# Optimization experiments

Hardware: AMD Instinct MI355X
Metric: run time of the kernel (lower is better)

Reference implementation:

```python
import jax, jax.numpy as jnp
import numpy as np

NEG_INF = -1e9
ROUTING_ITERS = 3


def squash(z):
    # z: [B, K, D]
    norm_sq = jnp.sum(z * z, axis=-1, keepdims=True)
    norm = jnp.sqrt(norm_sq + 1e-8)
    return norm_sq / (1.0 + norm_sq) * (z / norm)


def setup_inputs() -> dict:
    key = jax.random.key(0)
    k1, k2, k3, k4 = jax.random.split(key, 4)
    B, L, D, K = 2048, 200, 256, 8
    behavior_embeds = jax.random.normal(k1, (B, L, D), dtype=jnp.float32)
    W = jax.random.normal(k2, (D, D), dtype=jnp.float32) * (1.0 / np.sqrt(D))
    b_init = jax.random.normal(k3, (B, K, L), dtype=jnp.float32)
    mask = jax.random.randint(k4, (B, L), 0, 2, dtype=jnp.int32)
    return {"behavior_embeds": behavior_embeds, "W": W, "b_init": b_init, "mask": mask}


def reference(behavior_embeds, W, b_init, mask):
    # behavior_embeds: [B, L, D]; W: [D, D] (nn.Linear weight, y = x @ W.T)
    u_hat = jnp.einsum('bld,ed->ble', behavior_embeds, W)  # [B, L, D]
    # mask padding positions in routing logits
    b = jnp.where(mask[:, None, :] == 0, NEG_INF, b_init)  # [B, K, L]
    c = None
    for i in range(ROUTING_ITERS):
        w = jax.nn.softmax(b, axis=2)                      # [B, K, L]
        z = jnp.einsum('bkl,bld->bkd', w, u_hat)           # [B, K, D]
        c = squash(z)
        if i < ROUTING_ITERS - 1:
            b = b + jnp.einsum('bkd,bld->bkl', c, u_hat)
    return c
```

## Files before the change

### kernel.cpp

```cpp
#include <hip/hip_runtime.h>
#include <hip/hip_bf16.h>

#define B_ 2048
#define L_ 200
#define D_ 256
#define K_ 8

typedef __attribute__((ext_vector_type(8))) _Float16 half8;
typedef __attribute__((ext_vector_type(4))) _Float16 half4v;
typedef __attribute__((ext_vector_type(4))) float f32x4;

#define LTP 232
#define WP  232
#define CP  264

#define OFF_UTT  0
#define OFF_WH   118784
#define OFF_WL   126208
#define OFF_CH   133632
#define OFF_CL   142080
#define OFF_LB   150528
#define OFF_RED  156928
#define OFF_SC   157440
#define LDS_TOTAL 157472

__global__ __launch_bounds__(256) void w_to_f16(const float* __restrict__ W,
                                                _Float16* __restrict__ Wh) {
    const int idx = (blockIdx.x * 256 + threadIdx.x) * 4;
    const float4 v = *(const float4*)(W + idx);
    half4v h = { (_Float16)v.x, (_Float16)v.y, (_Float16)v.z, (_Float16)v.w };
    *(half4v*)(Wh + idx) = h;
}

__global__ __launch_bounds__(1024) void fused_mie(
        const float* __restrict__ X, const float* __restrict__ b_init,
        const int* __restrict__ mask, const _Float16* __restrict__ Wh,
        float* __restrict__ out) {
    extern __shared__ char dyn[];
    _Float16* utT = (_Float16*)(dyn + OFF_UTT);
    _Float16* wHs = (_Float16*)(dyn + OFF_WH);
    _Float16* wLs = (_Float16*)(dyn + OFF_WL);
    _Float16* cHs = (_Float16*)(dyn + OFF_CH);
    _Float16* cLs = (_Float16*)(dyn + OFF_CL);
    _Float16* Us  = (_Float16*)(dyn + OFF_CH);
    _Float16* Xs  = (_Float16*)(dyn + OFF_CL);
    float* lb   = (float*)(dyn + OFF_LB);
    float* red2 = (float*)(dyn + OFF_RED);
    float* scS  = (float*)(dyn + OFF_SC);

    const int b = blockIdx.x;
    const int t = threadIdx.x;
    const int w = t >> 6, lane = t & 63;
    const int fr = lane & 15, hi = lane >> 4;

    {
        const int row = t >> 2, part = t & 3;
        *(int4*)&utT[row * LTP + 200 + 8 * part] = make_int4(0, 0, 0, 0);
    }
    if (t < 928) *(int4*)(dyn + OFF_WH + 16 * t) = make_int4(0, 0, 0, 0);
    for (int idx = t; idx < K_ * L_; idx += 1024) {
        const int k = idx / L_, l = idx - k * L_;
        lb[idx] = (mask[b * L_ + l] == 0) ? -1e9f
                                          : b_init[(size_t)b * (K_ * L_) + idx];
    }

    half8 bw[8];
    {
        const _Float16* wr = Wh + (size_t)(16 * w + fr) * 256;
#pragma unroll
        for (int d0 = 0; d0 < 8; ++d0)
            bw[d0] = *(const half8*)(wr + 32 * d0 + 8 * hi);
    }

    const float* Xb = X + (size_t)b * L_ * D_;
    const int sc4 = lane * 4;
    {
        const float4 v = *(const float4*)(Xb + w * 256 + sc4);
        half4v h = { (_Float16)v.x, (_Float16)v.y, (_Float16)v.z, (_Float16)v.w };
        *(half4v*)&Xs[w * CP + sc4] = h;
    }
    __syncthreads();

    half8 au[8];
    for (int lt = 0; lt < 13; ++lt) {
        f32x4 acc = {};
#pragma unroll
        for (int d0 = 0; d0 < 8; ++d0) {
            const half8 a8 = *(const half8*)&Xs[fr * CP + 32 * d0 + 8 * hi];
            acc = __builtin_amdgcn_mfma_f32_16x16x32_f16(a8, bw[d0], acc, 0, 0, 0);
        }
        float4 xv = make_float4(0.f, 0.f, 0.f, 0.f);
        if (lt < 12) {
            const int l = 16 * (lt + 1) + w;
            if (l < L_) xv = *(const float4*)(Xb + l * 256 + sc4);
        }
#pragma unroll
        for (int j = 0; j < 4; ++j)
            Us[(4 * hi + j) * CP + 16 * w + fr] = (_Float16)acc[j];
        __syncthreads();
        if (w == lt) {
#pragma unroll
            for (int d0 = 0; d0 < 8; ++d0)
                au[d0] = *(const half8*)&Us[fr * CP + 32 * d0 + 8 * hi];
        }
        {
            const int c = t & 255, r0 = (t >> 8) * 4;
            half4v p = { Us[(r0 + 0) * CP + c], Us[(r0 + 1) * CP + c],
                         Us[(r0 + 2) * CP + c], Us[(r0 + 3) * CP + c] };
            *(half4v*)&utT[c * LTP + 16 * lt + r0] = p;
        }
        if (lt < 12) {
            half4v h = { (_Float16)xv.x, (_Float16)xv.y, (_Float16)xv.z, (_Float16)xv.w };
            *(half4v*)&Xs[w * CP + sc4] = h;
        }
        __syncthreads();
    }

    for (int iter = 0; iter < 3; ++iter) {
        if (t < 512) {
            const int k = t >> 6, ln = t & 63;
            float v[4];
            float m = -1e30f;
#pragma unroll
            for (int i = 0; i < 4; ++i) {
                const int l = ln + 64 * i;
                v[i] = (l < L_) ? lb[k * L_ + l] : -1e30f;
                m = fmaxf(m, v[i]);
            }
#pragma unroll
            for (int off = 32; off >= 1; off >>= 1)
                m = fmaxf(m, __shfl_xor(m, off));
            float e[4], s = 0.f;
#pragma unroll
            for (int i = 0; i < 4; ++i) {
                const int l = ln + 64 * i;
                e[i] = (l < L_) ? __expf(v[i] - m) : 0.f;
                s += e[i];
            }
#pragma unroll
            for (int off = 32; off >= 1; off >>= 1)
                s += __shfl_xor(s, off);
            const float rinv = 1.0f / s;
#pragma unroll
            for (int i = 0; i < 4; ++i) {
                const int l = ln + 64 * i;
                if (l < L_) {
                    const float wv = e[i] * rinv;
                    const _Float16 h = (_Float16)wv;
                    wHs[k * WP + l] = h;
                    wLs[k * WP + l] = (_Float16)(wv - (float)h);
                }
            }
        }
        __syncthreads();

        f32x4 zac = {};
#pragma unroll
        for (int ks = 0; ks < 7; ++ks) {
            const half8 bz = *(const half8*)&utT[(16 * w + fr) * LTP + 32 * ks + 8 * hi];
            const half8 ah = *(const half8*)&wHs[fr * WP + 32 * ks + 8 * hi];
            const half8 al = *(const half8*)&wLs[fr * WP + 32 * ks + 8 * hi];
            zac = __builtin_amdgcn_mfma_f32_16x16x32_f16(ah, bz, zac, 0, 0, 0);
            zac = __builtin_amdgcn_mfma_f32_16x16x32_f16(al, bz, zac, 0, 0, 0);
        }

        float sq0 = zac[0] * zac[0], sq1 = zac[1] * zac[1];
        float sq2 = zac[2] * zac[2], sq3 = zac[3] * zac[3];
#pragma unroll
        for (int off = 1; off <= 8; off <<= 1) {
            sq0 += __shfl_xor(sq0, off);
            sq1 += __shfl_xor(sq1, off);
            sq2 += __shfl_xor(sq2, off);
            sq3 += __shfl_xor(sq3, off);
        }
        if (fr == 0 && hi < 2) {
            f32x4 sv = { sq0, sq1, sq2, sq3 };
            *(f32x4*)&red2[w * 8 + 4 * hi] = sv;
        }
        __syncthreads();
        if (t < 8) {
            float ns = 0.f;
#pragma unroll
            for (int ww = 0; ww < 16; ++ww) ns += red2[ww * 8 + t];
            scS[t] = ns / ((1.f + ns) * sqrtf(ns + 1e-8f));
        }
        __syncthreads();

        if (iter == 2) {
            if (hi < 2) {
                const f32x4 sc = *(const f32x4*)&scS[4 * hi];
                float* op = out + (size_t)b * (K_ * D_) + (4 * hi) * D_ + 16 * w + fr;
#pragma unroll
                for (int j = 0; j < 4; ++j) op[j * D_] = sc[j] * zac[j];
            }
        } else {
            if (hi < 2) {
                const f32x4 sc = *(const f32x4*)&scS[4 * hi];
#pragma unroll
                for (int j = 0; j < 4; ++j) {
                    const float v = sc[j] * zac[j];
                    const _Float16 h = (_Float16)v;
                    cHs[(4 * hi + j) * CP + 16 * w + fr] = h;
                    cLs[(4 * hi + j) * CP + 16 * w + fr] = (_Float16)(v - (float)h);
                }
            }
            __syncthreads();

            if (w < 13) {
                f32x4 dac = {};
#pragma unroll
                for (int d0 = 0; d0 < 8; ++d0) {
                    const half8 bh = *(const half8*)&cHs[fr * CP + 32 * d0 + 8 * hi];
                    const half8 bl = *(const half8*)&cLs[fr * CP + 32 * d0 + 8 * hi];
                    dac = __builtin_amdgcn_mfma_f32_16x16x32_f16(au[d0], bh, dac, 0, 0, 0);
                    dac = __builtin_amdgcn_mfma_f32_16x16x32_f16(au[d0], bl, dac, 0, 0, 0);
                }
                if (fr < 8) {
#pragma unroll
                    for (int j = 0; j < 4; ++j) {
                        const int l = 16 * w + 4 * hi + j;
                        if (l < L_) lb[fr * L_ + l] += dac[j];
                    }
                }
            }
            __syncthreads();
        }
    }
}

extern "C" void kernel_launch(void* const* d_in, const int* in_sizes, int n_in,
                              void* d_out, int out_size, void* d_ws, size_t ws_size,
                              hipStream_t stream) {
    (void)in_sizes; (void)n_in; (void)out_size; (void)ws_size;
    const float* behavior = (const float*)d_in[0];
    const float* W        = (const float*)d_in[1];
    const float* b_init   = (const float*)d_in[2];
    const int*   mask     = (const int*)d_in[3];
    float* out      = (float*)d_out;
    _Float16* Wh    = (_Float16*)d_ws;

    hipFuncSetAttribute((const void*)fused_mie,
                        hipFuncAttributeMaxDynamicSharedMemorySize, LDS_TOTAL);

    w_to_f16<<<64, 256, 0, stream>>>(W, Wh);
    fused_mie<<<B_, 1024, LDS_TOTAL, stream>>>(behavior, b_init, mask, Wh, out);
}
```

Measured before the change: 264.3 us.

## Double-buffer X tiles and write transposed projection directly to LDS

The projection loop now double-buffers the X staging tile, which drops one barrier per iteration. Swapping the MFMA operands yields the transposed result, so the U tile is written straight into utT without the intermediate Us buffer and its transpose pass. The per-wave au fragments are gathered from utT after the loop using scalar strided LDS reads. The aim is to cut barriers and LDS traffic in the projection phase, at the cost of strided 2-byte stores and gathers that may cause bank conflicts.

```diff
diff --git a/kernel.cpp b/kernel.cpp
--- a/kernel.cpp
+++ b/kernel.cpp
@@ -17,8 +17,8 @@
 #define OFF_UTT  0
 #define OFF_WH   118784
 #define OFF_WL   126208
-#define OFF_CH   133632
-#define OFF_CL   142080
+#define OFF_XA   133632
+#define OFF_XB   142080
 #define OFF_LB   150528
 #define OFF_RED  156928
 #define OFF_SC   157440
@@ -32,7 +32,7 @@
     *(half4v*)(Wh + idx) = h;
 }
 
-__global__ __launch_bounds__(1024) void fused_mie(
+__global__ __launch_bounds__(1024) void fused_mie2(
         const float* __restrict__ X, const float* __restrict__ b_init,
         const int* __restrict__ mask, const _Float16* __restrict__ Wh,
         float* __restrict__ out) {
@@ -40,10 +40,10 @@
     _Float16* utT = (_Float16*)(dyn + OFF_UTT);
     _Float16* wHs = (_Float16*)(dyn + OFF_WH);
     _Float16* wLs = (_Float16*)(dyn + OFF_WL);
-    _Float16* cHs = (_Float16*)(dyn + OFF_CH);
-    _Float16* cLs = (_Float16*)(dyn + OFF_CL);
-    _Float16* Us  = (_Float16*)(dyn + OFF_CH);
-    _Float16* Xs  = (_Float16*)(dyn + OFF_CL);
+    _Float16* XsA = (_Float16*)(dyn + OFF_XA);
+    _Float16* XsB = (_Float16*)(dyn + OFF_XB);
+    _Float16* cHs = (_Float16*)(dyn + OFF_XA);
+    _Float16* cLs = (_Float16*)(dyn + OFF_XB);
     float* lb   = (float*)(dyn + OFF_LB);
     float* red2 = (float*)(dyn + OFF_RED);
     float* scS  = (float*)(dyn + OFF_SC);
@@ -77,43 +77,44 @@
     {
         const float4 v = *(const float4*)(Xb + w * 256 + sc4);
         half4v h = { (_Float16)v.x, (_Float16)v.y, (_Float16)v.z, (_Float16)v.w };
-        *(half4v*)&Xs[w * CP + sc4] = h;
+        *(half4v*)&XsA[w * CP + sc4] = h;
     }
     __syncthreads();
 
-    half8 au[8];
     for (int lt = 0; lt < 13; ++lt) {
-        f32x4 acc = {};
-#pragma unroll
-        for (int d0 = 0; d0 < 8; ++d0) {
-            const half8 a8 = *(const half8*)&Xs[fr * CP + 32 * d0 + 8 * hi];
-            acc = __builtin_amdgcn_mfma_f32_16x16x32_f16(a8, bw[d0], acc, 0, 0, 0);
-        }
+        _Float16* cur = (lt & 1) ? XsB : XsA;
+        _Float16* nxt = (lt & 1) ? XsA : XsB;
         float4 xv = make_float4(0.f, 0.f, 0.f, 0.f);
         if (lt < 12) {
             const int l = 16 * (lt + 1) + w;
             if (l < L_) xv = *(const float4*)(Xb + l * 256 + sc4);
         }
+        f32x4 acc = {};
+#pragma unroll
+        for (int d0 = 0; d0 < 8; ++d0) {
+            const half8 a8 = *(const half8*)&cur[fr * CP + 32 * d0 + 8 * hi];
+            acc = __builtin_amdgcn_mfma_f32_16x16x32_f16(bw[d0], a8, acc, 0, 0, 0);
+        }
 #pragma unroll
         for (int j = 0; j < 4; ++j)
-            Us[(4 * hi + j) * CP + 16 * w + fr] = (_Float16)acc[j];
-        __syncthreads();
-        if (w == lt) {
-#pragma unroll
-            for (int d0 = 0; d0 < 8; ++d0)
-                au[d0] = *(const half8*)&Us[fr * CP + 32 * d0 + 8 * hi];
-        }
-        {
-            const int c = t & 255, r0 = (t >> 8) * 4;
-            half4v p = { Us[(r0 + 0) * CP + c], Us[(r0 + 1) * CP + c],
-                         Us[(r0 + 2) * CP + c], Us[(r0 + 3) * CP + c] };
-            *(half4v*)&utT[c * LTP + 16 * lt + r0] = p;
-        }
+            utT[(16 * w + 4 * hi + j) * LTP + 16 * lt + fr] = (_Float16)acc[j];
         if (lt < 12) {
             half4v h = { (_Float16)xv.x, (_Float16)xv.y, (_Float16)xv.z, (_Float16)xv.w };
-            *(half4v*)&Xs[w * CP + sc4] = h;
-        }
-        __syncthreads();
+            *(half4v*)&nxt[w * CP + sc4] = h;
+        }
+        __syncthreads();
+    }
+
+    half8 au[8];
+    if (w < 13) {
+#pragma unroll
+        for (int d0 = 0; d0 < 8; ++d0) {
+            _Float16 tmp[8];
+#pragma unroll
+            for (int j = 0; j < 8; ++j)
+                tmp[j] = utT[(32 * d0 + 8 * hi + j) * LTP + 16 * w + fr];
+            au[d0] = *(half8*)tmp;
+        }
     }
 
     for (int iter = 0; iter < 3; ++iter) {
@@ -239,9 +240,9 @@
     float* out      = (float*)d_out;
     _Float16* Wh    = (_Float16*)d_ws;
 
-    hipFuncSetAttribute((const void*)fused_mie,
+    hipFuncSetAttribute((const void*)fused_mie2,
                         hipFuncAttributeMaxDynamicSharedMemorySize, LDS_TOTAL);
 
     w_to_f16<<<64, 256, 0, stream>>>(W, Wh);
-    fused_mie<<<B_, 1024, LDS_TOTAL, stream>>>(behavior, b_init, mask, Wh, out);
+    fused_mie2<<<B_, 1024, LDS_TOTAL, stream>>>(behavior, b_init, mask, Wh, out);
 }
```

After: 264.8 us. Within noise of the previous version (+0.2%).
